# Optimization experiments

Measured on AMD Instinct MI355X. Metric: run time of the kernel, lower is better.

The kernel has to match this reference:

```python
import jax, jax.numpy as jnp
import numpy as np

N = 100000   # num nodes
E = 640000   # num edges
IN, H, OUT = 6, 128, 1
BN_EPS = 1e-5


def setup_inputs() -> dict:
    key = jax.random.key(0)
    ks = jax.random.split(key, 12)
    x = jax.random.normal(ks[0], (N, IN), dtype=jnp.float32)
    edge_index = jax.random.randint(ks[1], (2, E), 0, N, dtype=jnp.int64)
    def lin(k, fin, fout):
        s = 1.0 / np.sqrt(fin)
        return jax.random.uniform(k, (fin, fout), jnp.float32, -s, s)
    return {
        "x": x,
        "edge_index": edge_index,
        "W1": lin(ks[2], IN, H),  "b1": jnp.zeros((H,), jnp.float32),
        "W2": lin(ks[3], H, H),   "b2": jnp.zeros((H,), jnp.float32),
        "W3": lin(ks[4], H, OUT), "b3": jnp.zeros((OUT,), jnp.float32),
        "g1": jnp.ones((H,), jnp.float32),  "be1": jnp.zeros((H,), jnp.float32),
        "g2": jnp.ones((H,), jnp.float32),  "be2": jnp.zeros((H,), jnp.float32),
    }


def _gcn_norm(edge_index):
    # add self-loops, then symmetric normalization D^-1/2 (A+I) D^-1/2
    loop = jnp.arange(N, dtype=edge_index.dtype)
    src = jnp.concatenate([edge_index[0], loop])
    dst = jnp.concatenate([edge_index[1], loop])
    deg = jax.ops.segment_sum(jnp.ones_like(dst, dtype=jnp.float32), dst, num_segments=N)
    dis = jnp.where(deg > 0, jax.lax.rsqrt(deg), 0.0)
    norm = dis[src] * dis[dst]  # (E+N,)
    return src, dst, norm


def _conv(h, W, b, src, dst, norm):
    m = h @ W                                   # (N, out) linear transform first
    msg = m[src] * norm[:, None]                # gather + edge scaling
    return jax.ops.segment_sum(msg, dst, num_segments=N) + b


def _bn(h, g, be):
    mu = h.mean(axis=0)
    var = h.var(axis=0)  # biased, as torch BN uses for normalization
    return g * (h - mu) * jax.lax.rsqrt(var + BN_EPS) + be


def reference(x, edge_index, W1, b1, W2, b2, W3, b3, g1, be1, g2, be2):
    src, dst, norm = _gcn_norm(edge_index)
    h = jax.nn.relu(_bn(_conv(x, W1, b1, src, dst, norm), g1, be1))
    h = jax.nn.relu(_bn(_conv(h, W2, b2, src, dst, norm), g2, be2))
    out = _conv(h, W3, b3, src, dst, norm)
    return jax.nn.sigmoid(out)  # (N, 1) risk scores
```

## Files before the change

kernel.cpp:

```cpp
#include <hip/hip_runtime.h>
#include <hip/hip_bf16.h>
#include <math.h>

#define HDIM 128
#define BN_EPS 1e-5f
#define CHUNK 512
#define TM 64
#define LDA 132

__device__ __forceinline__ int eget(const void* ei, long long pos, int is64) {
    return is64 ? (int)((const long long*)ei)[pos] : ((const int*)ei)[pos];
}
__device__ __forceinline__ unsigned short f2bf(float f) {
    unsigned int u = __float_as_uint(f);
    u += 0x7fffu + ((u >> 16) & 1u);
    return (unsigned short)(u >> 16);
}
__device__ __forceinline__ unsigned int pack2bf(float lo, float hi) {
    return (unsigned int)f2bf(lo) | ((unsigned int)f2bf(hi) << 16);
}
__device__ __forceinline__ float bflo(unsigned int u) {
    return __uint_as_float(u << 16);
}
__device__ __forceinline__ float bfhi(unsigned int u) {
    return __uint_as_float(u & 0xffff0000u);
}

__global__ void k_detect(const int* ei32, int* flag) {
    if (threadIdx.x == 0) {
        int nz = 0;
        for (int k = 0; k < 64; ++k) nz += (ei32[2 * k + 1] != 0);
        *flag = (nz < 8) ? 1 : 0;
    }
}

__global__ void k_count(const void* ei, const int* flag, int* cnt, int E) {
    int e = blockIdx.x * blockDim.x + threadIdx.x;
    if (e < E) {
        int d = eget(ei, (long long)E + e, *flag);
        atomicAdd(&cnt[d], 1);
    }
}

__global__ void k_dis(const int* cnt, float* dis, int N) {
    int i = blockIdx.x * blockDim.x + threadIdx.x;
    if (i < N) dis[i] = rsqrtf((float)(cnt[i] + 1));
}

__global__ void k_scan1(const int* cnt, int* bsum, int N) {
    __shared__ int s[256];
    int t = threadIdx.x;
    int i = blockIdx.x * CHUNK + t;
    int v = 0;
    if (i < N) v += cnt[i];
    if (i + 256 < N && t + 256 < CHUNK) v += cnt[i + 256];
    s[t] = v; __syncthreads();
    for (int o = 128; o > 0; o >>= 1) {
        if (t < o) s[t] += s[t + o];
        __syncthreads();
    }
    if (t == 0) bsum[blockIdx.x] = s[0];
}

__global__ void k_scan2(int* bsum, int nb) {
    __shared__ int s[512];
    int t = threadIdx.x;
    int carry = 0;
    for (int base = 0; base < nb; base += 512) {
        int i = base + t;
        int v = (i < nb) ? bsum[i] : 0;
        s[t] = v; __syncthreads();
        for (int o = 1; o < 512; o <<= 1) {
            int add = (t >= o) ? s[t - o] : 0;
            __syncthreads();
            s[t] += add;
            __syncthreads();
        }
        if (i < nb) bsum[i] = carry + s[t] - v;
        carry += s[511];
        __syncthreads();
    }
}

__global__ void k_scan3(int* cnt, const int* bsum, int* rowptr, int N) {
    __shared__ int s[CHUNK];
    int t = threadIdx.x;
    int i = blockIdx.x * CHUNK + t;
    int v = (i < N) ? cnt[i] : 0;
    s[t] = v; __syncthreads();
    for (int o = 1; o < CHUNK; o <<= 1) {
        int add = (t >= o) ? s[t - o] : 0;
        __syncthreads();
        s[t] += add;
        __syncthreads();
    }
    if (i < N) { rowptr[i] = bsum[blockIdx.x] + s[t] - v; cnt[i] = 0; }
    if (i == N - 1) rowptr[N] = bsum[blockIdx.x] + s[t];
}

__global__ void k_fillcsr(const void* ei, const int* flag, const float* dis,
                          const int* rowptr, int* fill, int2* emeta, int E) {
    int e = blockIdx.x * blockDim.x + threadIdx.x;
    if (e < E) {
        int is64 = *flag;
        int s = eget(ei, e, is64);
        int d = eget(ei, (long long)E + e, is64);
        int pos = rowptr[d] + atomicAdd(&fill[d], 1);
        emeta[pos] = make_int2(s, __float_as_int(dis[s] * dis[d]));
    }
}

__global__ void k_padx(const float* __restrict__ x, float* __restrict__ xp, int N) {
    int t = blockIdx.x * blockDim.x + threadIdx.x;
    if (t < N * 8) {
        int i = t >> 3, c = t & 7;
        xp[t] = (c < 6) ? x[i * 6 + c] : 0.f;
    }
}

__global__ void k_gath_x(const float* __restrict__ xp, const int* __restrict__ rowptr,
                         const int2* __restrict__ emeta,
                         const float* __restrict__ dis, float* __restrict__ aggx, int N) {
    int i = blockIdx.x * blockDim.x + threadIdx.x;
    if (i >= N) return;
    float d = dis[i], d2 = d * d;
    float4 A = *(const float4*)&xp[i * 8];
    float2 B = *(const float2*)&xp[i * 8 + 4];
    float a0 = A.x * d2, a1 = A.y * d2, a2 = A.z * d2;
    float a3 = A.w * d2, a4 = B.x * d2, a5 = B.y * d2;
    int p = rowptr[i], pe = rowptr[i + 1];
    for (; p + 4 <= pe; p += 4) {
        int2 e0 = emeta[p], e1 = emeta[p + 1], e2 = emeta[p + 2], e3 = emeta[p + 3];
        float n0 = __int_as_float(e0.y), n1 = __int_as_float(e1.y);
        float n2 = __int_as_float(e2.y), n3 = __int_as_float(e3.y);
        float4 A0 = *(const float4*)&xp[e0.x * 8];
        float2 B0 = *(const float2*)&xp[e0.x * 8 + 4];
        float4 A1 = *(const float4*)&xp[e1.x * 8];
        float2 B1 = *(const float2*)&xp[e1.x * 8 + 4];
        float4 A2 = *(const float4*)&xp[e2.x * 8];
        float2 B2 = *(const float2*)&xp[e2.x * 8 + 4];
        float4 A3 = *(const float4*)&xp[e3.x * 8];
        float2 B3 = *(const float2*)&xp[e3.x * 8 + 4];
        a0 += (A0.x * n0 + A1.x * n1) + (A2.x * n2 + A3.x * n3);
        a1 += (A0.y * n0 + A1.y * n1) + (A2.y * n2 + A3.y * n3);
        a2 += (A0.z * n0 + A1.z * n1) + (A2.z * n2 + A3.z * n3);
        a3 += (A0.w * n0 + A1.w * n1) + (A2.w * n2 + A3.w * n3);
        a4 += (B0.x * n0 + B1.x * n1) + (B2.x * n2 + B3.x * n3);
        a5 += (B0.y * n0 + B1.y * n1) + (B2.y * n2 + B3.y * n3);
    }
    for (; p < pe; ++p) {
        int2 e0 = emeta[p];
        float n0 = __int_as_float(e0.y);
        float4 A0 = *(const float4*)&xp[e0.x * 8];
        float2 B0 = *(const float2*)&xp[e0.x * 8 + 4];
        a0 += A0.x * n0; a1 += A0.y * n0; a2 += A0.z * n0;
        a3 += A0.w * n0; a4 += B0.x * n0; a5 += B0.y * n0;
    }
    aggx[i * 6 + 0] = a0; aggx[i * 6 + 1] = a1; aggx[i * 6 + 2] = a2;
    aggx[i * 6 + 3] = a3; aggx[i * 6 + 4] = a4; aggx[i * 6 + 5] = a5;
}

__global__ void k_gemm6(const float* __restrict__ aggx, const float* __restrict__ W1,
                        const float* __restrict__ b1, unsigned short* __restrict__ out,
                        float* __restrict__ S, int N) {
    __shared__ float w[6 * HDIM];
    __shared__ float bb[HDIM];
    __shared__ float sh1[256], sh2[256];
    for (int t = threadIdx.x; t < 6 * HDIM; t += blockDim.x) w[t] = W1[t];
    if (threadIdx.x < HDIM) bb[threadIdx.x] = b1[threadIdx.x];
    __syncthreads();
    int j = threadIdx.x & (HDIM - 1);
    int sub = threadIdx.x >> 7;
    float s1 = 0.f, s2 = 0.f;
    for (long long i = blockIdx.x * 2 + sub; i < N; i += (long long)gridDim.x * 2) {
        const float* r = &aggx[i * 6];
        float acc = bb[j];
        acc += r[0] * w[0 * HDIM + j];
        acc += r[1] * w[1 * HDIM + j];
        acc += r[2] * w[2 * HDIM + j];
        acc += r[3] * w[3 * HDIM + j];
        acc += r[4] * w[4 * HDIM + j];
        acc += r[5] * w[5 * HDIM + j];
        out[i * HDIM + j] = f2bf(acc);
        s1 += acc; s2 += acc * acc;
    }
    sh1[threadIdx.x] = s1; sh2[threadIdx.x] = s2;
    __syncthreads();
    if (threadIdx.x < HDIM) {
        atomicAdd(&S[j], sh1[j] + sh1[j + HDIM]);
        atomicAdd(&S[HDIM + j], sh2[j] + sh2[j + HDIM]);
    }
}

__global__ __launch_bounds__(512, 6)
void k_agg_gemm(const unsigned short* __restrict__ m1,
                const float* __restrict__ S1, const float* __restrict__ g1,
                const float* __restrict__ be1, float invN,
                const int* __restrict__ rowptr, const int2* __restrict__ emeta,
                const float* __restrict__ dis,
                const float* __restrict__ W, const float* __restrict__ b,
                unsigned short* __restrict__ out, float* __restrict__ S,
                int* __restrict__ ticket, int ntiles, int N) {
    __shared__ float At[TM * LDA];
    __shared__ float Pp[256];
    __shared__ int s_tile;
    const int tid = threadIdx.x;

    if (tid < HDIM) {
        float mu = S1[tid] * invN;
        float var = S1[HDIM + tid] * invN - mu * mu;
        float al = g1[tid] * rsqrtf(var + BN_EPS);
        Pp[tid] = al;
        Pp[HDIM + tid] = be1[tid] - mu * al;
    }
    __syncthreads();

    const int gl = tid & 15;
    const int gq = tid >> 4;
    const int c8 = gl * 8;
    const float4 pa0 = *(const float4*)&Pp[c8];
    const float4 pa1 = *(const float4*)&Pp[c8 + 4];
    const float4 pb0 = *(const float4*)&Pp[HDIM + c8];
    const float4 pb1 = *(const float4*)&Pp[HDIM + c8 + 4];

    const int cg = tid & 31;
    const int rg = tid >> 5;
    const int c0 = cg * 4;
    const int r0 = rg * 4;
    const float4 bv = *(const float4*)&b[c0];

    for (;;) {
        if (tid == 0) s_tile = atomicAdd(ticket, 1);
        __syncthreads();
        const int tile = s_tile;
        if (tile >= ntiles) return;
        const long long i0 = (long long)tile * TM;

        for (int nn = gq; nn < TM; nn += 32) {
            long long i = i0 + nn;
            float a0 = 0.f, a1 = 0.f, a2 = 0.f, a3 = 0.f;
            float a4 = 0.f, a5 = 0.f, a6 = 0.f, a7 = 0.f;
            if (i < N) {
                float d = dis[i], d2 = d * d;
                uint4 us = *(const uint4*)&m1[i * HDIM + c8];
                a0 = fmaxf(fmaf(pa0.x, bflo(us.x), pb0.x), 0.f) * d2;
                a1 = fmaxf(fmaf(pa0.y, bfhi(us.x), pb0.y), 0.f) * d2;
                a2 = fmaxf(fmaf(pa0.z, bflo(us.y), pb0.z), 0.f) * d2;
                a3 = fmaxf(fmaf(pa0.w, bfhi(us.y), pb0.w), 0.f) * d2;
                a4 = fmaxf(fmaf(pa1.x, bflo(us.z), pb1.x), 0.f) * d2;
                a5 = fmaxf(fmaf(pa1.y, bfhi(us.z), pb1.y), 0.f) * d2;
                a6 = fmaxf(fmaf(pa1.z, bflo(us.w), pb1.z), 0.f) * d2;
                a7 = fmaxf(fmaf(pa1.w, bfhi(us.w), pb1.w), 0.f) * d2;
                int p = rowptr[i], pe = rowptr[i + 1];
                for (; p + 2 <= pe; p += 2) {
                    int2 eA = emeta[p], eB = emeta[p + 1];
                    float nA = __int_as_float(eA.y), nB = __int_as_float(eB.y);
                    uint4 uA = *(const uint4*)&m1[(long long)eA.x * HDIM + c8];
                    uint4 uB = *(const uint4*)&m1[(long long)eB.x * HDIM + c8];
                    a0 += fmaxf(fmaf(pa0.x, bflo(uA.x), pb0.x), 0.f) * nA
                        + fmaxf(fmaf(pa0.x, bflo(uB.x), pb0.x), 0.f) * nB;
                    a1 += fmaxf(fmaf(pa0.y, bfhi(uA.x), pb0.y), 0.f) * nA
                        + fmaxf(fmaf(pa0.y, bfhi(uB.x), pb0.y), 0.f) * nB;
                    a2 += fmaxf(fmaf(pa0.z, bflo(uA.y), pb0.z), 0.f) * nA
                        + fmaxf(fmaf(pa0.z, bflo(uB.y), pb0.z), 0.f) * nB;
                    a3 += fmaxf(fmaf(pa0.w, bfhi(uA.y), pb0.w), 0.f) * nA
                        + fmaxf(fmaf(pa0.w, bfhi(uB.y), pb0.w), 0.f) * nB;
                    a4 += fmaxf(fmaf(pa1.x, bflo(uA.z), pb1.x), 0.f) * nA
                        + fmaxf(fmaf(pa1.x, bflo(uB.z), pb1.x), 0.f) * nB;
                    a5 += fmaxf(fmaf(pa1.y, bfhi(uA.z), pb1.y), 0.f) * nA
                        + fmaxf(fmaf(pa1.y, bfhi(uB.z), pb1.y), 0.f) * nB;
                    a6 += fmaxf(fmaf(pa1.z, bflo(uA.w), pb1.z), 0.f) * nA
                        + fmaxf(fmaf(pa1.z, bflo(uB.w), pb1.z), 0.f) * nB;
                    a7 += fmaxf(fmaf(pa1.w, bfhi(uA.w), pb1.w), 0.f) * nA
                        + fmaxf(fmaf(pa1.w, bfhi(uB.w), pb1.w), 0.f) * nB;
                }
                if (p < pe) {
                    int2 eA = emeta[p];
                    float nA = __int_as_float(eA.y);
                    uint4 uA = *(const uint4*)&m1[(long long)eA.x * HDIM + c8];
                    a0 += fmaxf(fmaf(pa0.x, bflo(uA.x), pb0.x), 0.f) * nA;
                    a1 += fmaxf(fmaf(pa0.y, bfhi(uA.x), pb0.y), 0.f) * nA;
                    a2 += fmaxf(fmaf(pa0.z, bflo(uA.y), pb0.z), 0.f) * nA;
                    a3 += fmaxf(fmaf(pa0.w, bfhi(uA.y), pb0.w), 0.f) * nA;
                    a4 += fmaxf(fmaf(pa1.x, bflo(uA.z), pb1.x), 0.f) * nA;
                    a5 += fmaxf(fmaf(pa1.y, bfhi(uA.z), pb1.y), 0.f) * nA;
                    a6 += fmaxf(fmaf(pa1.z, bflo(uA.w), pb1.z), 0.f) * nA;
                    a7 += fmaxf(fmaf(pa1.w, bfhi(uA.w), pb1.w), 0.f) * nA;
                }
            }
            *(float4*)&At[nn * LDA + c8]     = make_float4(a0, a1, a2, a3);
            *(float4*)&At[nn * LDA + c8 + 4] = make_float4(a4, a5, a6, a7);
        }
        __syncthreads();

        float acc[4][4];
        #pragma unroll
        for (int rr = 0; rr < 4; ++rr) {
            acc[rr][0] = bv.x; acc[rr][1] = bv.y; acc[rr][2] = bv.z; acc[rr][3] = bv.w;
        }
        for (int k = 0; k < HDIM; k += 4) {
            const float4 w0 = *(const float4*)&W[(k + 0) * HDIM + c0];
            const float4 w1 = *(const float4*)&W[(k + 1) * HDIM + c0];
            const float4 w2 = *(const float4*)&W[(k + 2) * HDIM + c0];
            const float4 w3 = *(const float4*)&W[(k + 3) * HDIM + c0];
            #pragma unroll
            for (int rr = 0; rr < 4; ++rr) {
                const float4 av = *(const float4*)&At[(r0 + rr) * LDA + k];
                acc[rr][0] = fmaf(av.x, w0.x, acc[rr][0]);
                acc[rr][1] = fmaf(av.x, w0.y, acc[rr][1]);
                acc[rr][2] = fmaf(av.x, w0.z, acc[rr][2]);
                acc[rr][3] = fmaf(av.x, w0.w, acc[rr][3]);
                acc[rr][0] = fmaf(av.y, w1.x, acc[rr][0]);
                acc[rr][1] = fmaf(av.y, w1.y, acc[rr][1]);
                acc[rr][2] = fmaf(av.y, w1.z, acc[rr][2]);
                acc[rr][3] = fmaf(av.y, w1.w, acc[rr][3]);
                acc[rr][0] = fmaf(av.z, w2.x, acc[rr][0]);
                acc[rr][1] = fmaf(av.z, w2.y, acc[rr][1]);
                acc[rr][2] = fmaf(av.z, w2.z, acc[rr][2]);
                acc[rr][3] = fmaf(av.z, w2.w, acc[rr][3]);
                acc[rr][0] = fmaf(av.w, w3.x, acc[rr][0]);
                acc[rr][1] = fmaf(av.w, w3.y, acc[rr][1]);
                acc[rr][2] = fmaf(av.w, w3.z, acc[rr][2]);
                acc[rr][3] = fmaf(av.w, w3.w, acc[rr][3]);
            }
        }

        float cs1[4] = {0.f, 0.f, 0.f, 0.f};
        float cs2[4] = {0.f, 0.f, 0.f, 0.f};
        #pragma unroll
        for (int rr = 0; rr < 4; ++rr) {
            long long i = i0 + r0 + rr;
            if (i < N) {
                uint2 o;
                o.x = pack2bf(acc[rr][0], acc[rr][1]);
                o.y = pack2bf(acc[rr][2], acc[rr][3]);
                *(uint2*)&out[i * HDIM + c0] = o;
                #pragma unroll
                for (int cc = 0; cc < 4; ++cc) {
                    float v = acc[rr][cc];
                    cs1[cc] += v; cs2[cc] += v * v;
                }
            }
        }
        __syncthreads();
        #pragma unroll
        for (int cc = 0; cc < 4; ++cc) {
            At[rg * HDIM + c0 + cc]        = cs1[cc];
            At[2048 + rg * HDIM + c0 + cc] = cs2[cc];
        }
        __syncthreads();
        if (tid < 256) {
            int j = tid & (HDIM - 1);
            int which = tid >> 7;
            const float* bp = &At[which * 2048 + j];
            float s = 0.f;
            #pragma unroll
            for (int g = 0; g < 16; ++g) s += bp[g * HDIM];
            atomicAdd(&S[which * HDIM + j], s);
        }
        __syncthreads();
    }
}

__global__ void k_gemv2(const unsigned short* __restrict__ m2,
                        const float* __restrict__ S2, const float* __restrict__ g2,
                        const float* __restrict__ be2, float invN,
                        const float* __restrict__ W3, float* __restrict__ m3, int N) {
    __shared__ float Pp[256];
    int tid = threadIdx.x;
    if (tid < HDIM) {
        float mu = S2[tid] * invN;
        float var = S2[HDIM + tid] * invN - mu * mu;
        float al = g2[tid] * rsqrtf(var + BN_EPS);
        Pp[tid] = al;
        Pp[HDIM + tid] = be2[tid] - mu * al;
    }
    __syncthreads();
    int l = tid & 31;
    int c4 = l * 4;
    float4 pa = *(const float4*)&Pp[c4];
    float4 pb = *(const float4*)&Pp[HDIM + c4];
    float4 w  = *(const float4*)&W3[c4];
    for (long long row = blockIdx.x * 8 + (tid >> 5); row < N;
         row += (long long)gridDim.x * 8) {
        uint2 v = *(const uint2*)&m2[row * HDIM + c4];
        float s = fmaxf(fmaf(pa.x, bflo(v.x), pb.x), 0.f) * w.x
                + fmaxf(fmaf(pa.y, bfhi(v.x), pb.y), 0.f) * w.y
                + fmaxf(fmaf(pa.z, bflo(v.y), pb.z), 0.f) * w.z
                + fmaxf(fmaf(pa.w, bfhi(v.y), pb.w), 0.f) * w.w;
        for (int o = 16; o > 0; o >>= 1) s += __shfl_down(s, o, 32);
        if (l == 0) m3[row] = s;
    }
}

__global__ void k_gath_o(const float* __restrict__ m3, const int* __restrict__ rowptr,
                         const int2* __restrict__ emeta,
                         const float* __restrict__ dis, const float* __restrict__ b3,
                         float* __restrict__ out, int N) {
    int i = blockIdx.x * blockDim.x + threadIdx.x;
    if (i < N) {
        float d = dis[i];
        float acc = m3[i] * d * d;
        int p = rowptr[i], pe = rowptr[i + 1];
        for (; p + 4 <= pe; p += 4) {
            int2 e0 = emeta[p], e1 = emeta[p + 1], e2 = emeta[p + 2], e3 = emeta[p + 3];
            float v0 = m3[e0.x] * __int_as_float(e0.y);
            float v1 = m3[e1.x] * __int_as_float(e1.y);
            float v2 = m3[e2.x] * __int_as_float(e2.y);
            float v3 = m3[e3.x] * __int_as_float(e3.y);
            acc += (v0 + v1) + (v2 + v3);
        }
        for (; p < pe; ++p) {
            int2 e0 = emeta[p];
            acc += m3[e0.x] * __int_as_float(e0.y);
        }
        acc += b3[0];
        out[i] = 1.f / (1.f + expf(-acc));
    }
}

extern "C" void kernel_launch(void* const* d_in, const int* in_sizes, int n_in,
                              void* d_out, int out_size, void* d_ws, size_t ws_size,
                              hipStream_t stream) {
    const float* x  = (const float*)d_in[0];
    const void*  ei = d_in[1];
    const float* W1 = (const float*)d_in[2];
    const float* b1 = (const float*)d_in[3];
    const float* W2 = (const float*)d_in[4];
    const float* b2 = (const float*)d_in[5];
    const float* W3 = (const float*)d_in[6];
    const float* b3 = (const float*)d_in[7];
    const float* g1 = (const float*)d_in[8];
    const float* be1 = (const float*)d_in[9];
    const float* g2 = (const float*)d_in[10];
    const float* be2 = (const float*)d_in[11];

    const int N = in_sizes[0] / 6;
    const int E = in_sizes[1] / 2;
    const float invN = 1.0f / (float)N;

    float* ws = (float*)d_ws;
    long long off = 0;
    auto pad4 = [](long long v) { return (v + 3) & ~3LL; };
    int*   flag   = (int*)ws;                 off += 16;
    int*   ticket = (int*)ws + 1;
    float* S1     = ws + off;                 off += 256;
    float* S2     = ws + off;                 off += 256;
    float* dis    = ws + off;                 off = pad4(off + N);
    int*   cnt    = (int*)(ws + off);         off = pad4(off + N);
    int*   rowptr = (int*)(ws + off);         off = pad4(off + N + 16);
    int2*  emeta  = (int2*)(ws + off);        off = pad4(off + (long long)2 * E);
    int*   bsum   = (int*)(ws + off);         off += 512;
    float* xp     = ws + off;                 off = pad4(off + (long long)8 * N);
    float* aggx   = ws + off;                 off = pad4(off + (long long)6 * N);
    float* m3     = ws + off;                 off = pad4(off + N);
    unsigned short* m1 = (unsigned short*)(ws + off); off = pad4(off + (long long)64 * N);
    unsigned short* m2 = (unsigned short*)(ws + off); off = pad4(off + (long long)64 * N);

    const int T = 256;
    const int bN  = (N + T - 1) / T;
    const int bE  = (E + T - 1) / T;
    const int nchunk = (N + CHUNK - 1) / CHUNK;
    const int ntiles = (N + TM - 1) / TM;

    hipMemsetAsync(ws, 0, 528 * sizeof(float), stream);
    hipMemsetAsync(cnt, 0, (size_t)N * sizeof(int), stream);
    k_detect<<<1, 64, 0, stream>>>((const int*)ei, flag);
    k_count<<<bE, T, 0, stream>>>(ei, flag, cnt, E);
    k_dis<<<bN, T, 0, stream>>>(cnt, dis, N);
    k_scan1<<<nchunk, 256, 0, stream>>>(cnt, bsum, N);
    k_scan2<<<1, 512, 0, stream>>>(bsum, nchunk);
    k_scan3<<<nchunk, CHUNK, 0, stream>>>(cnt, bsum, rowptr, N);
    k_fillcsr<<<bE, T, 0, stream>>>(ei, flag, dis, rowptr, cnt, emeta, E);

    k_padx<<<(N * 8 + T - 1) / T, T, 0, stream>>>(x, xp, N);
    k_gath_x<<<bN, T, 0, stream>>>(xp, rowptr, emeta, dis, aggx, N);
    k_gemm6<<<512, T, 0, stream>>>(aggx, W1, b1, m1, S1, N);

    k_agg_gemm<<<1024, 512, 0, stream>>>(m1, S1, g1, be1, invN,
                                         rowptr, emeta, dis,
                                         W2, b2, m2, S2, ticket, ntiles, N);

    k_gemv2<<<1024, T, 0, stream>>>(m2, S2, g2, be2, invN, W3, m3, N);
    k_gath_o<<<bN, T, 0, stream>>>(m3, rowptr, emeta, dis, b3, (float*)d_out, N);
}
```

Measured before the change: 278.7 us.

## Shrink agg-GEMM tiles to 32 rows with 256-thread blocks and 4-wide gathers

Halves the row tile and the block size of the fused aggregate+GEMM kernel, and doubles the grid. Each thread now gathers 4 bf16 features (8-byte loads) instead of 8, and the edge loop is unrolled by 4 so more independent gathers are in flight per thread. The aim is more resident waves and more memory-level parallelism for the irregular neighbor gathers. In exchange, the W tile is reused across fewer rows and there are more per-tile BN-statistic atomics.

```diff
diff --git a/kernel.cpp b/kernel.cpp
--- a/kernel.cpp
+++ b/kernel.cpp
@@ -5,7 +5,7 @@
 #define HDIM 128
 #define BN_EPS 1e-5f
 #define CHUNK 512
-#define TM 64
+#define TM 32
 #define LDA 132
 
 __device__ __forceinline__ int eget(const void* ei, long long pos, int is64) {
@@ -192,7 +192,7 @@
     }
 }
 
-__global__ __launch_bounds__(512, 6)
+__global__ __launch_bounds__(256, 8)
 void k_agg_gemm(const unsigned short* __restrict__ m1,
                 const float* __restrict__ S1, const float* __restrict__ g1,
                 const float* __restrict__ be1, float invN,
@@ -215,13 +215,11 @@
     }
     __syncthreads();
 
-    const int gl = tid & 15;
-    const int gq = tid >> 4;
-    const int c8 = gl * 8;
-    const float4 pa0 = *(const float4*)&Pp[c8];
-    const float4 pa1 = *(const float4*)&Pp[c8 + 4];
-    const float4 pb0 = *(const float4*)&Pp[HDIM + c8];
-    const float4 pb1 = *(const float4*)&Pp[HDIM + c8 + 4];
+    const int gl = tid & 31;
+    const int gq = tid >> 5;
+    const int c4 = gl * 4;
+    const float4 pa = *(const float4*)&Pp[c4];
+    const float4 pb = *(const float4*)&Pp[HDIM + c4];
 
     const int cg = tid & 31;
     const int rg = tid >> 5;
@@ -236,60 +234,69 @@
         if (tile >= ntiles) return;
         const long long i0 = (long long)tile * TM;
 
-        for (int nn = gq; nn < TM; nn += 32) {
+        for (int nn = gq; nn < TM; nn += 8) {
             long long i = i0 + nn;
             float a0 = 0.f, a1 = 0.f, a2 = 0.f, a3 = 0.f;
-            float a4 = 0.f, a5 = 0.f, a6 = 0.f, a7 = 0.f;
             if (i < N) {
                 float d = dis[i], d2 = d * d;
-                uint4 us = *(const uint4*)&m1[i * HDIM + c8];
-                a0 = fmaxf(fmaf(pa0.x, bflo(us.x), pb0.x), 0.f) * d2;
-                a1 = fmaxf(fmaf(pa0.y, bfhi(us.x), pb0.y), 0.f) * d2;
-                a2 = fmaxf(fmaf(pa0.z, bflo(us.y), pb0.z), 0.f) * d2;
-                a3 = fmaxf(fmaf(pa0.w, bfhi(us.y), pb0.w), 0.f) * d2;
-                a4 = fmaxf(fmaf(pa1.x, bflo(us.z), pb1.x), 0.f) * d2;
-                a5 = fmaxf(fmaf(pa1.y, bfhi(us.z), pb1.y), 0.f) * d2;
-                a6 = fmaxf(fmaf(pa1.z, bflo(us.w), pb1.z), 0.f) * d2;
-                a7 = fmaxf(fmaf(pa1.w, bfhi(us.w), pb1.w), 0.f) * d2;
+                uint2 us = *(const uint2*)&m1[i * HDIM + c4];
+                a0 = fmaxf(fmaf(pa.x, bflo(us.x), pb.x), 0.f) * d2;
+                a1 = fmaxf(fmaf(pa.y, bfhi(us.x), pb.y), 0.f) * d2;
+                a2 = fmaxf(fmaf(pa.z, bflo(us.y), pb.z), 0.f) * d2;
+                a3 = fmaxf(fmaf(pa.w, bfhi(us.y), pb.w), 0.f) * d2;
                 int p = rowptr[i], pe = rowptr[i + 1];
-                for (; p + 2 <= pe; p += 2) {
+                for (; p + 4 <= pe; p += 4) {
+                    int2 eA = emeta[p],     eB = emeta[p + 1];
+                    int2 eC = emeta[p + 2], eD = emeta[p + 3];
+                    float nA = __int_as_float(eA.y), nB = __int_as_float(eB.y);
+                    float nC = __int_as_float(eC.y), nD = __int_as_float(eD.y);
+                    uint2 uA = *(const uint2*)&m1[(long long)eA.x * HDIM + c4];
+                    uint2 uB = *(const uint2*)&m1[(long long)eB.x * HDIM + c4];
+                    uint2 uC = *(const uint2*)&m1[(long long)eC.x * HDIM + c4];
+                    uint2 uD = *(const uint2*)&m1[(long long)eD.x * HDIM + c4];
+                    a0 += (fmaxf(fmaf(pa.x, bflo(uA.x), pb.x), 0.f) * nA
+                         + fmaxf(fmaf(pa.x, bflo(uB.x), pb.x), 0.f) * nB)
+                        + (fmaxf(fmaf(pa.x, bflo(uC.x), pb.x), 0.f) * nC
+                         + fmaxf(fmaf(pa.x, bflo(uD.x), pb.x), 0.f) * nD);
+                    a1 += (fmaxf(fmaf(pa.y, bfhi(uA.x), pb.y), 0.f) * nA
+                         + fmaxf(fmaf(pa.y, bfhi(uB.x), pb.y), 0.f) * nB)
+                        + (fmaxf(fmaf(pa.y, bfhi(uC.x), pb.y), 0.f) * nC
+                         + fmaxf(fmaf(pa.y, bfhi(uD.x), pb.y), 0.f) * nD);
+                    a2 += (fmaxf(fmaf(pa.z, bflo(uA.y), pb.z), 0.f) * nA
+                         + fmaxf(fmaf(pa.z, bflo(uB.y), pb.z), 0.f) * nB)
+                        + (fmaxf(fmaf(pa.z, bflo(uC.y), pb.z), 0.f) * nC
+                         + fmaxf(fmaf(pa.z, bflo(uD.y), pb.z), 0.f) * nD);
+                    a3 += (fmaxf(fmaf(pa.w, bfhi(uA.y), pb.w), 0.f) * nA
+                         + fmaxf(fmaf(pa.w, bfhi(uB.y), pb.w), 0.f) * nB)
+                        + (fmaxf(fmaf(pa.w, bfhi(uC.y), pb.w), 0.f) * nC
+                         + fmaxf(fmaf(pa.w, bfhi(uD.y), pb.w), 0.f) * nD);
+                }
+                if (p + 2 <= pe) {
                     int2 eA = emeta[p], eB = emeta[p + 1];
                     float nA = __int_as_float(eA.y), nB = __int_as_float(eB.y);
-                    uint4 uA = *(const uint4*)&m1[(long long)eA.x * HDIM + c8];
-                    uint4 uB = *(const uint4*)&m1[(long long)eB.x * HDIM + c8];
-                    a0 += fmaxf(fmaf(pa0.x, bflo(uA.x), pb0.x), 0.f) * nA
-                        + fmaxf(fmaf(pa0.x, bflo(uB.x), pb0.x), 0.f) * nB;
-                    a1 += fmaxf(fmaf(pa0.y, bfhi(uA.x), pb0.y), 0.f) * nA
-                        + fmaxf(fmaf(pa0.y, bfhi(uB.x), pb0.y), 0.f) * nB;
-                    a2 += fmaxf(fmaf(pa0.z, bflo(uA.y), pb0.z), 0.f) * nA
-                        + fmaxf(fmaf(pa0.z, bflo(uB.y), pb0.z), 0.f) * nB;
-                    a3 += fmaxf(fmaf(pa0.w, bfhi(uA.y), pb0.w), 0.f) * nA
-                        + fmaxf(fmaf(pa0.w, bfhi(uB.y), pb0.w), 0.f) * nB;
-                    a4 += fmaxf(fmaf(pa1.x, bflo(uA.z), pb1.x), 0.f) * nA
-                        + fmaxf(fmaf(pa1.x, bflo(uB.z), pb1.x), 0.f) * nB;
-                    a5 += fmaxf(fmaf(pa1.y, bfhi(uA.z), pb1.y), 0.f) * nA
-                        + fmaxf(fmaf(pa1.y, bfhi(uB.z), pb1.y), 0.f) * nB;
-                    a6 += fmaxf(fmaf(pa1.z, bflo(uA.w), pb1.z), 0.f) * nA
-                        + fmaxf(fmaf(pa1.z, bflo(uB.w), pb1.z), 0.f) * nB;
-                    a7 += fmaxf(fmaf(pa1.w, bfhi(uA.w), pb1.w), 0.f) * nA
-                        + fmaxf(fmaf(pa1.w, bfhi(uB.w), pb1.w), 0.f) * nB;
+                    uint2 uA = *(const uint2*)&m1[(long long)eA.x * HDIM + c4];
+                    uint2 uB = *(const uint2*)&m1[(long long)eB.x * HDIM + c4];
+                    a0 += fmaxf(fmaf(pa.x, bflo(uA.x), pb.x), 0.f) * nA
+                        + fmaxf(fmaf(pa.x, bflo(uB.x), pb.x), 0.f) * nB;
+                    a1 += fmaxf(fmaf(pa.y, bfhi(uA.x), pb.y), 0.f) * nA
+                        + fmaxf(fmaf(pa.y, bfhi(uB.x), pb.y), 0.f) * nB;
+                    a2 += fmaxf(fmaf(pa.z, bflo(uA.y), pb.z), 0.f) * nA
+                        + fmaxf(fmaf(pa.z, bflo(uB.y), pb.z), 0.f) * nB;
+                    a3 += fmaxf(fmaf(pa.w, bfhi(uA.y), pb.w), 0.f) * nA
+                        + fmaxf(fmaf(pa.w, bfhi(uB.y), pb.w), 0.f) * nB;
+                    p += 2;
                 }
                 if (p < pe) {
                     int2 eA = emeta[p];
                     float nA = __int_as_float(eA.y);
-                    uint4 uA = *(const uint4*)&m1[(long long)eA.x * HDIM + c8];
-                    a0 += fmaxf(fmaf(pa0.x, bflo(uA.x), pb0.x), 0.f) * nA;
-                    a1 += fmaxf(fmaf(pa0.y, bfhi(uA.x), pb0.y), 0.f) * nA;
-                    a2 += fmaxf(fmaf(pa0.z, bflo(uA.y), pb0.z), 0.f) * nA;
-                    a3 += fmaxf(fmaf(pa0.w, bfhi(uA.y), pb0.w), 0.f) * nA;
-                    a4 += fmaxf(fmaf(pa1.x, bflo(uA.z), pb1.x), 0.f) * nA;
-                    a5 += fmaxf(fmaf(pa1.y, bfhi(uA.z), pb1.y), 0.f) * nA;
-                    a6 += fmaxf(fmaf(pa1.z, bflo(uA.w), pb1.z), 0.f) * nA;
-                    a7 += fmaxf(fmaf(pa1.w, bfhi(uA.w), pb1.w), 0.f) * nA;
+                    uint2 uA = *(const uint2*)&m1[(long long)eA.x * HDIM + c4];
+                    a0 += fmaxf(fmaf(pa.x, bflo(uA.x), pb.x), 0.f) * nA;
+                    a1 += fmaxf(fmaf(pa.y, bfhi(uA.x), pb.y), 0.f) * nA;
+                    a2 += fmaxf(fmaf(pa.z, bflo(uA.y), pb.z), 0.f) * nA;
+                    a3 += fmaxf(fmaf(pa.w, bfhi(uA.y), pb.w), 0.f) * nA;
                 }
             }
-            *(float4*)&At[nn * LDA + c8]     = make_float4(a0, a1, a2, a3);
-            *(float4*)&At[nn * LDA + c8 + 4] = make_float4(a4, a5, a6, a7);
+            *(float4*)&At[nn * LDA + c4] = make_float4(a0, a1, a2, a3);
         }
         __syncthreads();
 
@@ -346,16 +353,16 @@
         #pragma unroll
         for (int cc = 0; cc < 4; ++cc) {
             At[rg * HDIM + c0 + cc]        = cs1[cc];
-            At[2048 + rg * HDIM + c0 + cc] = cs2[cc];
-        }
-        __syncthreads();
-        if (tid < 256) {
+            At[1024 + rg * HDIM + c0 + cc] = cs2[cc];
+        }
+        __syncthreads();
+        {
             int j = tid & (HDIM - 1);
             int which = tid >> 7;
-            const float* bp = &At[which * 2048 + j];
+            const float* bp = &At[which * 1024 + j];
             float s = 0.f;
             #pragma unroll
-            for (int g = 0; g < 16; ++g) s += bp[g * HDIM];
+            for (int g = 0; g < 8; ++g) s += bp[g * HDIM];
             atomicAdd(&S[which * HDIM + j], s);
         }
         __syncthreads();
@@ -477,7 +484,7 @@
     k_gath_x<<<bN, T, 0, stream>>>(xp, rowptr, emeta, dis, aggx, N);
     k_gemm6<<<512, T, 0, stream>>>(aggx, W1, b1, m1, S1, N);
 
-    k_agg_gemm<<<1024, 512, 0, stream>>>(m1, S1, g1, be1, invN,
+    k_agg_gemm<<<2048, 256, 0, stream>>>(m1, S1, g1, be1, invN,
                                          rowptr, emeta, dis,
                                          W2, b2, m2, S2, ticket, ntiles, N);
 
```

Measured after the change: 364.7 us. 1.31x slower.
